# Kernel tuning notes

Hardware: AMD Instinct MI355X
Metric: run time of the kernel (lower is better)

The kernel has to match this reference:

```python
import jax, jax.numpy as jnp
import numpy as np

N_NODES = 40000
N_EDGES = 640000
FEAT_IN = 128
EDGE_FEAT_IN = 16
HID = 128
N_LAYERS = 4
NUM_GRAPHS = 256


def _linear_params(key, fan_in, fan_out):
    k1, k2 = jax.random.split(key)
    s = 1.0 / np.sqrt(fan_in)
    W = jax.random.uniform(k1, (fan_in, fan_out), jnp.float32, -s, s)
    b = jax.random.uniform(k2, (fan_out,), jnp.float32, -s, s)
    return W, b


def setup_inputs() -> dict:
    key = jax.random.key(0)
    ks = jax.random.split(key, 8)
    h = jax.random.normal(ks[0], (N_NODES, FEAT_IN), jnp.float32)
    e = jax.random.normal(ks[1], (N_EDGES, EDGE_FEAT_IN), jnp.float32)
    edge_index = jax.random.randint(ks[2], (2, N_EDGES), 0, N_NODES, jnp.int32)
    batch = jnp.sort(jax.random.randint(ks[3], (N_NODES,), 0, NUM_GRAPHS, jnp.int32))

    W_embed, b_embed = _linear_params(ks[4], FEAT_IN, HID)
    W_eembed, b_eembed = _linear_params(ks[5], EDGE_FEAT_IN, HID)

    layer_keys = jax.random.split(ks[6], N_LAYERS * 3)
    Wm_l, bm_l, Wh_l, bh_l, We_l, be_l = [], [], [], [], [], []
    for i in range(N_LAYERS):
        Wm, bm = _linear_params(layer_keys[3 * i + 0], 3 * HID, HID)
        Wh, bh = _linear_params(layer_keys[3 * i + 1], 2 * HID, HID)
        We, be = _linear_params(layer_keys[3 * i + 2], 3 * HID, HID)
        Wm_l.append(Wm); bm_l.append(bm)
        Wh_l.append(Wh); bh_l.append(bh)
        We_l.append(We); be_l.append(be)

    return {
        "h": h, "e": e, "edge_index": edge_index, "batch": batch,
        "W_embed": W_embed, "b_embed": b_embed,
        "W_eembed": W_eembed, "b_eembed": b_eembed,
        "Wm": jnp.stack(Wm_l), "bm": jnp.stack(bm_l),
        "Wh": jnp.stack(Wh_l), "bh": jnp.stack(bh_l),
        "We": jnp.stack(We_l), "be": jnp.stack(be_l),
    }


def reference(h, e, W_embed, b_embed, W_eembed, b_eembed,
              Wm, bm, Wh, bh, We, be, edge_index, batch):
    send, rec = edge_index[0], edge_index[1]
    h = h @ W_embed + b_embed          # [N, H]
    e = e @ W_eembed + b_eembed        # [E, H]

    def layer(carry, params):
        h, e = carry
        Wm_i, bm_i, Wh_i, bh_i, We_i, be_i = params
        h_send = h[send]               # [E, H] gather
        h_rec = h[rec]                 # [E, H] gather
        cat3 = jnp.concatenate([h_send, h_rec, e], axis=1)  # [E, 3H]
        messages = cat3 @ Wm_i + bm_i                        # [E, H]
        agg = jax.ops.segment_sum(messages, rec, num_segments=N_NODES)  # scatter_add
        h_new = jnp.concatenate([h, agg], axis=1) @ Wh_i + bh_i
        # NOTE: e_update uses h_send/h_rec from the OLD h, as in the source.
        e_new = cat3 @ We_i + be_i
        return (h_new, e_new), None

    (h, e), _ = jax.lax.scan(layer, (h, e), (Wm, bm, Wh, bh, We, be))
    return jax.ops.segment_sum(h, batch, num_segments=NUM_GRAPHS)  # global_add_pool
```

## Files before the change

### kernel.cpp

```cpp
#include <hip/hip_runtime.h>
#include <hip/hip_bf16.h>

#define NN 40000
#define NE 640000
#define NG 256
#define EW 48

typedef __attribute__((ext_vector_type(8))) short bf16x8;
typedef __attribute__((ext_vector_type(4))) float f32x4;

__device__ __forceinline__ unsigned f2b_u(float f){
  unsigned u = __builtin_bit_cast(unsigned, f);
  u += 0x7fffu + ((u >> 16) & 1u);
  return u >> 16;
}
__device__ __forceinline__ float b2f(unsigned short h){
  unsigned u = ((unsigned)h) << 16;
  return __builtin_bit_cast(float, u);
}
__device__ __forceinline__ unsigned scale_pk(unsigned u, float dg){
  float lo = __builtin_bit_cast(float, u << 16);
  float hi = __builtin_bit_cast(float, u & 0xffff0000u);
  return f2b_u(lo * dg) | (f2b_u(hi * dg) << 16);
}

#define LSTRIDE 147456

__global__ __launch_bounds__(256) void pack2_k(
    const float* __restrict__ Wembed, const float* __restrict__ Wh,
    const float* __restrict__ We, unsigned short* __restrict__ wt,
    unsigned short* __restrict__ wp)
{
  __shared__ float T[64][65];
  const int bx = blockIdx.x;
  const int tx = threadIdx.x & 63, ty = threadIdx.x >> 6;
  const float* src; unsigned short* dst; int rowbase, stride, koff, jt, kt;
  if (bx < 4){
    src = Wembed; dst = wt; rowbase = 0; stride = 128; koff = 0;
    kt = bx & 1; jt = bx >> 1;
  } else {
    const int q = bx - 4, l = q / 24, w = q % 24;
    unsigned short* base = wt + 16384 + (size_t)l * LSTRIDE;
    const float* wh = Wh + (size_t)l * 256 * 128;
    const float* we = We + (size_t)l * 384 * 128;
    if (w < 4){       src = wh; rowbase = 0;   dst = base;          stride = 640; koff = 0;   kt = w & 1;        jt = w >> 1; }
    else if (w < 12){ const int u = w - 4;  src = we; rowbase = 128; dst = base + 81920;  stride = 256; koff = 0;   kt = u & 3; jt = u >> 2; }
    else if (w < 16){ const int u = w - 12; src = we; rowbase = 0;   dst = base + 114688; stride = 256; koff = 0;   kt = u & 1; jt = u >> 1; }
    else if (w < 20){ const int u = w - 16; src = we; rowbase = 256; dst = base + 114688; stride = 256; koff = 128; kt = u & 1; jt = u >> 1; }
    else {            const int u = w - 20; src = wh; rowbase = 128; dst = wp + l * 16384; stride = 128; koff = 0; kt = u & 1; jt = u >> 1; }
  }
  const int k0 = kt * 64, j0 = jt * 64;
  #pragma unroll
  for (int rr = 0; rr < 16; ++rr){
    const int r = ty + rr * 4;
    T[r][tx] = src[(size_t)(rowbase + k0 + r) * 128 + j0 + tx];
  }
  __syncthreads();
  #pragma unroll
  for (int rr = 0; rr < 16; ++rr){
    const int j = ty + rr * 4;
    dst[(size_t)(j0 + j) * stride + koff + k0 + tx] = (unsigned short)f2b_u(T[tx][j]);
  }
}

__global__ __launch_bounds__(256, 2) void prodg_k(
    const float* __restrict__ Wm, const unsigned short* __restrict__ wp,
    unsigned short* __restrict__ wt)
{
  __shared__ unsigned short As[128 * 128];
  __shared__ unsigned short Bs[128 * 128];
  const int l = blockIdx.x / 3, pi = blockIdx.x % 3;
  const int rowoff = (pi == 0) ? 128 : (pi == 1) ? 0 : 256;
  const int poff   = (pi == 0) ? 128 : (pi == 1) ? 256 : 384;
  const float* Am = Wm + (size_t)l * 384 * 128 + (size_t)rowoff * 128;
  const unsigned short* Bt = wp + l * 16384;
  unsigned short* base = wt + 16384 + (size_t)l * LSTRIDE;

  const int tid = threadIdx.x;
  const int lane = tid & 63, wave = tid >> 6;
  const int qm = (wave & 1) << 6, qn = (wave >> 1) << 6;
  const int lr = lane & 15, lkc = lane >> 4;
  const int chunk = tid & 15, r0 = tid >> 4;
  f32x4 acc[4][4] = {};

  #pragma unroll
  for (int rr = 0; rr < 8; ++rr){
    const int r = r0 + rr * 16;
    const float* Af = Am + ((size_t)r << 7) + chunk * 8;
    const float4 f0 = *(const float4*)Af;
    const float4 f1 = *(const float4*)(Af + 4);
    uint4 va;
    va.x = f2b_u(f0.x) | (f2b_u(f0.y) << 16);
    va.y = f2b_u(f0.z) | (f2b_u(f0.w) << 16);
    va.z = f2b_u(f1.x) | (f2b_u(f1.y) << 16);
    va.w = f2b_u(f1.z) | (f2b_u(f1.w) << 16);
    *(uint4*)&As[r * 128 + ((chunk ^ (r & 7)) << 3)] = va;
    *(uint4*)&Bs[r * 128 + ((chunk ^ (r & 7)) << 3)] =
        *(const uint4*)(Bt + (size_t)r * 128 + chunk * 8);
  }
  __syncthreads();
  #pragma unroll
  for (int kk = 0; kk < 4; ++kk){
    const int kc = kk * 4 + lkc;
    bf16x8 af[4], bfr[4];
    #pragma unroll
    for (int mi = 0; mi < 4; ++mi){
      const int r = qm + mi * 16 + lr;
      af[mi] = *(const bf16x8*)&As[r * 128 + ((kc ^ (r & 7)) << 3)];
    }
    #pragma unroll
    for (int ni = 0; ni < 4; ++ni){
      const int r = qn + ni * 16 + lr;
      bfr[ni] = *(const bf16x8*)&Bs[r * 128 + ((kc ^ (r & 7)) << 3)];
    }
    #pragma unroll
    for (int mi = 0; mi < 4; ++mi)
      #pragma unroll
      for (int ni = 0; ni < 4; ++ni)
        acc[mi][ni] = __builtin_amdgcn_mfma_f32_16x16x32_bf16(af[mi], bfr[ni], acc[mi][ni], 0, 0, 0);
  }

  const int rbase = (lane >> 4) << 2;
  #pragma unroll
  for (int mi = 0; mi < 4; ++mi){
    #pragma unroll
    for (int r = 0; r < 4; ++r){
      const int gr = qm + mi * 16 + rbase + r;
      #pragma unroll
      for (int ni = 0; ni < 4; ++ni){
        const int col = qn + ni * 16 + lr;
        const unsigned short b = (unsigned short)f2b_u(acc[mi][ni][r]);
        base[(size_t)col * 640 + poff + gr] = b;
        if (pi == 2) base[(size_t)col * 640 + 512 + gr] = b;
      }
    }
  }
}

__global__ __launch_bounds__(1024, 1) void vec2b_k(
    const float* __restrict__ bm, const float* __restrict__ be,
    const unsigned short* __restrict__ wt, const unsigned short* __restrict__ wp,
    float* __restrict__ rw)
{
  __shared__ unsigned short s_wp[16384];
  __shared__ unsigned short s_m3[16384];
  __shared__ unsigned short s_w3[16384];
  __shared__ float c[128], cb[128];
  __shared__ float part_rw[128][8], part_cn[128][8];
  const int t = threadIdx.x;
  const int j = t >> 3, p = t & 7;
  if (t < 128) c[t] = 0.f;

  for (int l = 0; l < 4; ++l){
    const unsigned short* base = wt + 16384 + (size_t)l * LSTRIDE;
    ((uint4*)s_wp)[t]        = ((const uint4*)(wp + l * 16384))[t];
    ((uint4*)s_wp)[t + 1024] = ((const uint4*)(wp + l * 16384))[t + 1024];
    {
      const uint4* srcm = (const uint4*)(base + (size_t)j * 640 + 384);
      ((uint4*)(s_m3 + j * 128))[p * 2]     = srcm[p * 2];
      ((uint4*)(s_m3 + j * 128))[p * 2 + 1] = srcm[p * 2 + 1];
      const uint4* srcw = (const uint4*)(base + 114688 + (size_t)j * 256 + 128);
      ((uint4*)(s_w3 + j * 128))[p * 2]     = srcw[p * 2];
      ((uint4*)(s_w3 + j * 128))[p * 2 + 1] = srcw[p * 2 + 1];
    }
    if (t < 128) cb[t] = bm[l * 128 + t];
    __syncthreads();
    float prw = 0.f, pcn = 0.f;
    #pragma unroll
    for (int q = 0; q < 16; ++q){
      const int kk = p * 16 + q;
      prw += cb[kk] * b2f(s_wp[j * 128 + kk]) + c[kk] * b2f(s_m3[j * 128 + kk]);
      pcn += c[kk] * b2f(s_w3[j * 128 + kk]);
    }
    part_rw[j][p] = prw; part_cn[j][p] = pcn;
    __syncthreads();
    if (t < 128){
      float rwj = 0.f, cnj = be[l * 128 + t];
      #pragma unroll
      for (int i = 0; i < 8; ++i){ rwj += part_rw[t][i]; cnj += part_cn[t][i]; }
      rw[l * 128 + t] = rwj;
      __syncthreads();
      c[t] = cnj;
    } else {
      __syncthreads();
    }
    __syncthreads();
  }
}

struct YCfg {
  const void* A[5];
  const unsigned short* Bt;
  unsigned short* out0;
  const float* bias;
  const float* rv;
  int np;
  int bstride;
  int scale_mask;
};
struct GArgs { YCfg y[3]; };

template<int AT0>
__global__ __launch_bounds__(256, 2) void gemm_multi(
    GArgs ga, int M, const float* __restrict__ degf)
{
  __shared__ unsigned short As[128 * 128];
  __shared__ unsigned short Bs[128 * 128];
  const YCfg c = ga.y[blockIdx.y];
  const int tid = threadIdx.x;
  const int m0 = blockIdx.x * 128;
  const int lane = tid & 63, wave = tid >> 6;
  const int qm = (wave & 1) << 6, qn = (wave >> 1) << 6;
  const int lr = lane & 15, lkc = lane >> 4;
  const int chunk = tid & 15, r0 = tid >> 4;
  f32x4 acc[4][4] = {};

  for (int p = 0; p < c.np; ++p){
    if (p) __syncthreads();
    const unsigned short* Ab = (const unsigned short*)c.A[p];
    const bool scl = (c.scale_mask >> p) & 1;
    #pragma unroll
    for (int rr = 0; rr < 8; ++rr){
      const int r = r0 + rr * 16;
      const int gr = m0 + r;
      uint4 va = make_uint4(0u, 0u, 0u, 0u);
      if (gr < M){
        if (AT0 && p == 0){
          const float* Af = (const float*)c.A[0] + ((size_t)gr << 7) + chunk * 8;
          const float4 f0 = *(const float4*)Af;
          const float4 f1 = *(const float4*)(Af + 4);
          va.x = f2b_u(f0.x) | (f2b_u(f0.y) << 16);
          va.y = f2b_u(f0.z) | (f2b_u(f0.w) << 16);
          va.z = f2b_u(f1.x) | (f2b_u(f1.y) << 16);
          va.w = f2b_u(f1.z) | (f2b_u(f1.w) << 16);
        } else {
          va = *(const uint4*)(Ab + ((size_t)gr << 7) + chunk * 8);
          if (scl){
            const float dg = degf[gr];
            va.x = scale_pk(va.x, dg); va.y = scale_pk(va.y, dg);
            va.z = scale_pk(va.z, dg); va.w = scale_pk(va.w, dg);
          }
        }
      }
      *(uint4*)&As[r * 128 + ((chunk ^ (r & 7)) << 3)] = va;
      *(uint4*)&Bs[r * 128 + ((chunk ^ (r & 7)) << 3)] =
          *(const uint4*)(c.Bt + (size_t)r * c.bstride + p * 128 + chunk * 8);
    }
    __syncthreads();
    #pragma unroll
    for (int kk = 0; kk < 4; ++kk){
      const int kc = kk * 4 + lkc;
      bf16x8 af[4], bfr[4];
      #pragma unroll
      for (int mi = 0; mi < 4; ++mi){
        const int r = qm + mi * 16 + lr;
        af[mi] = *(const bf16x8*)&As[r * 128 + ((kc ^ (r & 7)) << 3)];
      }
      #pragma unroll
      for (int ni = 0; ni < 4; ++ni){
        const int r = qn + ni * 16 + lr;
        bfr[ni] = *(const bf16x8*)&Bs[r * 128 + ((kc ^ (r & 7)) << 3)];
      }
      #pragma unroll
      for (int mi = 0; mi < 4; ++mi)
        #pragma unroll
        for (int ni = 0; ni < 4; ++ni)
          acc[mi][ni] = __builtin_amdgcn_mfma_f32_16x16x32_bf16(af[mi], bfr[ni], acc[mi][ni], 0, 0, 0);
    }
  }

  const int rbase = (lane >> 4) << 2;
  #pragma unroll
  for (int mi = 0; mi < 4; ++mi){
    #pragma unroll
    for (int r = 0; r < 4; ++r){
      const int gr = m0 + qm + mi * 16 + rbase + r;
      if (gr >= M) continue;
      const size_t ro = (size_t)gr << 7;
      float dg = 0.f;
      if (c.rv) dg = degf[gr];
      #pragma unroll
      for (int ni = 0; ni < 4; ++ni){
        const int col = qn + ni * 16 + lr;
        float v = acc[mi][ni][r];
        if (c.bias) v += c.bias[col];
        if (c.rv)   v += dg * c.rv[col];
        c.out0[ro + col] = (unsigned short)f2b_u(v);
      }
    }
  }
}

__global__ void fill_ell_k(const int* __restrict__ rec, const int* __restrict__ send,
                           int* __restrict__ cnt, int2* __restrict__ ell){
  const int i = blockIdx.x * 256 + threadIdx.x;
  if (i < NE){
    const int r = rec[i];
    const int k = atomicAdd(&cnt[r], 1);
    if (k < EW) ell[r * EW + k] = make_int2(send[i], i);
  }
}

__global__ void aux_k(const int* __restrict__ cnt, float* __restrict__ degf,
                      const int* __restrict__ batch, int* __restrict__ gptr){
  const int b = blockIdx.x, t = threadIdx.x;
  if (b < 157){
    const int i = b * 256 + t;
    if (i < NN) degf[i] = (float)cnt[i];
  } else {
    if (t < NG){
      int lo = 0, hi = NN;
      while (lo < hi){
        const int mid = (lo + hi) >> 1;
        if (batch[mid] < t) lo = mid + 1; else hi = mid;
      }
      gptr[t] = lo;
      if (t == 0) gptr[NG] = NN;
    }
  }
}

__global__ __launch_bounds__(256) void sraw_s0_k(
    const int* __restrict__ cnt, const int2* __restrict__ ell,
    const float* __restrict__ e_in, const float* __restrict__ W,
    const float* __restrict__ bias, unsigned short* __restrict__ TPS)
{
  __shared__ float sums[16][16];
  __shared__ float dgs[16];
  __shared__ float Ws[2048];
  __shared__ float bs[128];
  const int t = threadIdx.x;
  const int n0 = blockIdx.x * 16;
  for (int i = t; i < 2048; i += 256) Ws[i] = W[i];
  if (t < 128) bs[t] = bias[t];
  {
    const int a = t >> 4, c16 = t & 15;
    const int n = n0 + a;
    const int m0 = cnt[n];
    const int m = (m0 < EW) ? m0 : EW;
    const int2* row = ell + n * EW;
    float acc = 0.f;
    int j = 0;
    for (; j + 2 <= m; j += 2){
      const int e0 = row[j].y, e1 = row[j + 1].y;
      acc += e_in[(size_t)e0 * 16 + c16] + e_in[(size_t)e1 * 16 + c16];
    }
    if (j < m) acc += e_in[(size_t)row[j].y * 16 + c16];
    sums[a][c16] = acc;
    if (c16 == 0) dgs[a] = (float)m0;
  }
  __syncthreads();
  #pragma unroll
  for (int i = 0; i < 8; ++i){
    const int o = t + 256 * i;
    const int node = o >> 7, col = o & 127;
    float acc = dgs[node] * bs[col];
    #pragma unroll
    for (int k = 0; k < 16; ++k) acc += sums[node][k] * Ws[k * 128 + col];
    TPS[((size_t)(n0 + node) << 7) + col] = (unsigned short)f2b_u(acc);
  }
}

__global__ __launch_bounds__(256) void gather_q_k(
    const int* __restrict__ cnt, const int2* __restrict__ ell,
    const unsigned short* __restrict__ hb, unsigned short* __restrict__ tb)
{
  const int pass = blockIdx.y;
  const int n = blockIdx.x * 4 + (threadIdx.x >> 6);
  const int lane = threadIdx.x & 63;
  const int grp = lane >> 4, l16 = lane & 15;
  const int mc = cnt[n];
  const int m = (mc < EW) ? mc : EW;
  const int idx = (lane < m) ? ell[n * EW + lane].x : 0;
  const unsigned short* cp = hb + pass * 32 + (l16 << 1);
  float a0 = 0.f, a1 = 0.f;
  for (int k = 0; k < m; k += 8){
    const int kk0 = k + grp, kk1 = k + 4 + grp;
    const int s0 = __shfl(idx, kk0 < m ? kk0 : 0);
    const int s1 = __shfl(idx, kk1 < m ? kk1 : 0);
    unsigned v0 = 0u, v1 = 0u;
    if (kk0 < m) v0 = *(const unsigned*)(cp + ((size_t)s0 << 7));
    if (kk1 < m) v1 = *(const unsigned*)(cp + ((size_t)s1 << 7));
    a0 += b2f((unsigned short)(v0 & 0xffffu)) + b2f((unsigned short)(v1 & 0xffffu));
    a1 += b2f((unsigned short)(v0 >> 16)) + b2f((unsigned short)(v1 >> 16));
  }
  a0 += __shfl_xor(a0, 16); a0 += __shfl_xor(a0, 32);
  a1 += __shfl_xor(a1, 16); a1 += __shfl_xor(a1, 32);
  if (grp == 0)
    *(unsigned*)(tb + ((size_t)n << 7) + pass * 32 + (l16 << 1)) =
        f2b_u(a0) | (f2b_u(a1) << 16);
}

__global__ void pool_k(const int* __restrict__ gptr, const unsigned short* __restrict__ hb,
                       float* __restrict__ out)
{
  const int g = blockIdx.x * 4 + (threadIdx.x >> 6);
  const int lane = threadIdx.x & 63;
  float a0 = 0.f, a1 = 0.f;
  for (int n = gptr[g]; n < gptr[g + 1]; ++n){
    const unsigned v = *(const unsigned*)(hb + ((size_t)n << 7) + 2 * lane);
    a0 += b2f((unsigned short)(v & 0xffffu));
    a1 += b2f((unsigned short)(v >> 16));
  }
  float2 r; r.x = a0; r.y = a1;
  *(float2*)(out + (size_t)g * 128 + 2 * lane) = r;
}

extern "C" void kernel_launch(void* const* d_in, const int* in_sizes, int n_in,
                              void* d_out, int out_size, void* d_ws, size_t ws_size,
                              hipStream_t stream)
{
  const float* h_in     = (const float*)d_in[0];
  const float* e_in     = (const float*)d_in[1];
  const int*   eidx     = (const int*)d_in[2];
  const int*   batch    = (const int*)d_in[3];
  const float* W_embed  = (const float*)d_in[4];
  const float* b_embed  = (const float*)d_in[5];
  const float* W_eembed = (const float*)d_in[6];
  const float* b_eembed = (const float*)d_in[7];
  const float* Wm       = (const float*)d_in[8];
  const float* bm       = (const float*)d_in[9];
  const float* Wh       = (const float*)d_in[10];
  const float* bh       = (const float*)d_in[11];
  const float* We       = (const float*)d_in[12];
  const float* be       = (const float*)d_in[13];
  const int* send = eidx;
  const int* rec  = eidx + NE;

  char* ws = (char*)d_ws;
  size_t off = 0;
  auto alloc = [&](size_t bytes) -> char* {
    char* p = ws + off;
    off = (off + bytes + 255) & ~(size_t)255;
    return p;
  };
  unsigned short* wt  = (unsigned short*)alloc((size_t)(16384 + 4 * LSTRIDE) * 2);
  unsigned short* wp  = (unsigned short*)alloc((size_t)4 * 16384 * 2);
  unsigned short* hA  = (unsigned short*)alloc((size_t)NN * 128 * 2);
  unsigned short* hB  = (unsigned short*)alloc((size_t)NN * 128 * 2);
  unsigned short* Q0  = (unsigned short*)alloc((size_t)NN * 128 * 2);
  unsigned short* Q1  = (unsigned short*)alloc((size_t)NN * 128 * 2);
  unsigned short* T0  = (unsigned short*)alloc((size_t)NN * 128 * 2);
  unsigned short* T1  = (unsigned short*)alloc((size_t)NN * 128 * 2);
  unsigned short* tb  = (unsigned short*)alloc((size_t)NN * 128 * 2);
  float* rw   = (float*)alloc((size_t)512 * 4);
  int* cnt    = (int*)alloc((size_t)NN * 4);
  float* degf = (float*)alloc((size_t)NN * 4);
  int* gptr   = (int*)alloc((size_t)(NG + 1) * 4);
  int2* ell   = (int2*)alloc((size_t)NN * EW * 8);

  if (off > ws_size) return;

  const dim3 B256(256);

  pack2_k<<<dim3(100), B256, 0, stream>>>(W_embed, Wh, We, wt, wp);
  prodg_k<<<dim3(12), B256, 0, stream>>>(Wm, wp, wt);
  vec2b_k<<<dim3(1), dim3(1024), 0, stream>>>(bm, be, wt, wp, rw);

  hipMemsetAsync(cnt, 0, (size_t)NN * 4, stream);
  fill_ell_k<<<dim3(2500), B256, 0, stream>>>(rec, send, cnt, ell);
  aux_k<<<dim3(158), B256, 0, stream>>>(cnt, degf, batch, gptr);
  sraw_s0_k<<<dim3(NN / 16), B256, 0, stream>>>(cnt, ell, e_in, W_eembed, b_eembed, T0);

  {
    GArgs ga = {};
    ga.y[0].A[0] = h_in; ga.y[0].Bt = wt; ga.y[0].out0 = hA;
    ga.y[0].bias = b_embed; ga.y[0].np = 1; ga.y[0].bstride = 128;
    ga.y[0].scale_mask = 0;
    gemm_multi<1><<<dim3(313, 1), B256, 0, stream>>>(ga, NN, degf);
  }

  unsigned short* hc = hA;  unsigned short* hn = hB;
  unsigned short* Qc = Q0;  unsigned short* Qn = Q1;
  unsigned short* Tc = T0;  unsigned short* Tn = T1;
  for (int l = 0; l < 4; ++l){
    const unsigned short* LB = wt + 16384 + (size_t)l * LSTRIDE;

    gather_q_k<<<dim3(NN / 4, 4), B256, 0, stream>>>(cnt, ell, hc, tb);

    GArgs ga = {};
    YCfg& y0 = ga.y[0];
    y0.A[0] = hc; y0.A[1] = hc; y0.A[2] = tb; y0.A[3] = Tc; y0.A[4] = Qc;
    y0.Bt = LB; y0.out0 = hn; y0.bias = bh + l * 128; y0.rv = rw + l * 128;
    y0.np = (l == 0) ? 4 : 5;
    y0.bstride = 640; y0.scale_mask = (1 << 1) | (1 << 4);
    int ny = 1;
    if (l < 3){
      YCfg& y1 = ga.y[1];
      y1.A[0] = hc; y1.A[1] = Qc; y1.Bt = LB + 81920;
      y1.out0 = Qn; y1.np = (l == 0) ? 1 : 2; y1.bstride = 256; y1.scale_mask = 0;
      YCfg& y2 = ga.y[2];
      y2.A[0] = tb; y2.A[1] = Tc; y2.Bt = LB + 114688;
      y2.out0 = Tn; y2.np = 2; y2.bstride = 256; y2.scale_mask = 0;
      ny = 3;
    }
    gemm_multi<0><<<dim3(313, ny), B256, 0, stream>>>(ga, NN, degf);

    unsigned short* t2;
    t2 = hc; hc = hn; hn = t2;
    t2 = Qc; Qc = Qn; Qn = t2;
    t2 = Tc; Tc = Tn; Tn = t2;
  }

  pool_k<<<dim3(NG / 4), B256, 0, stream>>>(gptr, hc, (float*)d_out);
}
```

Baseline: 697.2 us.

## Prearrange weights into MFMA fragment layout and drop shared-memory B staging

Adds a one-off kernel that copies weight panels into a fragment-ordered layout, so the GEMM reads B operands directly from global memory (L1/L2-resident) instead of staging them in LDS. Degree scaling of A tiles is replaced by a second accumulator for the same A tile, applied as dg*(acc2+rv) in the epilogue. This removes half the LDS footprint and the per-stage scale conversions, and cuts the number of A tile loads (hc loaded once for two weight blocks). In exchange, each wave issues global loads for B inside the MFMA loop, and a second accumulator array doubles accumulator register use, which can hurt occupancy.

Result: slower. 738.5 us (+5.9%).

```diff
diff --git a/kernel.cpp b/kernel.cpp
--- a/kernel.cpp
+++ b/kernel.cpp
@@ -17,11 +17,6 @@
 __device__ __forceinline__ float b2f(unsigned short h){
   unsigned u = ((unsigned)h) << 16;
   return __builtin_bit_cast(float, u);
-}
-__device__ __forceinline__ unsigned scale_pk(unsigned u, float dg){
-  float lo = __builtin_bit_cast(float, u << 16);
-  float hi = __builtin_bit_cast(float, u & 0xffff0000u);
-  return f2b_u(lo * dg) | (f2b_u(hi * dg) << 16);
 }
 
 #define LSTRIDE 147456
@@ -137,6 +132,26 @@
   }
 }
 
+__global__ void frag_k(const unsigned short* __restrict__ wt,
+                       unsigned short* __restrict__ wf)
+{
+  const int gp = blockIdx.y;
+  const int g = blockIdx.x * 256 + threadIdx.x;
+  const int kc = g >> 7, r = g & 127;
+  const unsigned short* src; unsigned short* dst; int bstride, p;
+  if (gp == 0){ src = wt; dst = wf; bstride = 128; p = 0; }
+  else {
+    const int q = gp - 1, l = q / 9, w = q % 9;
+    const unsigned short* sb = wt + 16384 + (size_t)l * LSTRIDE;
+    dst = wf + 16384 + (size_t)l * LSTRIDE + w * 16384;
+    if (w < 5){      src = sb;           bstride = 640; p = w; }
+    else if (w < 7){ src = sb + 81920;   bstride = 256; p = w - 5; }
+    else {           src = sb + 114688;  bstride = 256; p = w - 7; }
+  }
+  *(uint4*)(dst + (size_t)g * 8) =
+      *(const uint4*)(src + (size_t)r * bstride + p * 128 + kc * 8);
+}
+
 __global__ __launch_bounds__(1024, 1) void vec2b_k(
     const float* __restrict__ bm, const float* __restrict__ be,
     const unsigned short* __restrict__ wt, const unsigned short* __restrict__ wp,
@@ -188,24 +203,16 @@
   }
 }
 
-struct YCfg {
-  const void* A[5];
-  const unsigned short* Bt;
-  unsigned short* out0;
-  const float* bias;
-  const float* rv;
-  int np;
-  int bstride;
-  int scale_mask;
-};
+struct Stg { const void* A; int nb; int bo[2]; int bt[2]; };
+struct YCfg { Stg s[4]; int ns; unsigned short* out0; const float* bias; const float* rv; };
 struct GArgs { YCfg y[3]; };
 
 template<int AT0>
 __global__ __launch_bounds__(256, 2) void gemm_multi(
-    GArgs ga, int M, const float* __restrict__ degf)
+    GArgs ga, int M, const float* __restrict__ degf,
+    const unsigned short* __restrict__ wf)
 {
   __shared__ unsigned short As[128 * 128];
-  __shared__ unsigned short Bs[128 * 128];
   const YCfg c = ga.y[blockIdx.y];
   const int tid = threadIdx.x;
   const int m0 = blockIdx.x * 128;
@@ -213,20 +220,20 @@
   const int qm = (wave & 1) << 6, qn = (wave >> 1) << 6;
   const int lr = lane & 15, lkc = lane >> 4;
   const int chunk = tid & 15, r0 = tid >> 4;
-  f32x4 acc[4][4] = {};
-
-  for (int p = 0; p < c.np; ++p){
-    if (p) __syncthreads();
-    const unsigned short* Ab = (const unsigned short*)c.A[p];
-    const bool scl = (c.scale_mask >> p) & 1;
+  f32x4 ac1[4][4] = {};
+  f32x4 ac2[4][4] = {};
+
+  for (int s = 0; s < c.ns; ++s){
+    if (s) __syncthreads();
+    const Stg st = c.s[s];
     #pragma unroll
     for (int rr = 0; rr < 8; ++rr){
       const int r = r0 + rr * 16;
       const int gr = m0 + r;
       uint4 va = make_uint4(0u, 0u, 0u, 0u);
       if (gr < M){
-        if (AT0 && p == 0){
-          const float* Af = (const float*)c.A[0] + ((size_t)gr << 7) + chunk * 8;
+        if (AT0 && s == 0){
+          const float* Af = (const float*)st.A + ((size_t)gr << 7) + chunk * 8;
           const float4 f0 = *(const float4*)Af;
           const float4 f1 = *(const float4*)(Af + 4);
           va.x = f2b_u(f0.x) | (f2b_u(f0.y) << 16);
@@ -234,38 +241,40 @@
           va.z = f2b_u(f1.x) | (f2b_u(f1.y) << 16);
           va.w = f2b_u(f1.z) | (f2b_u(f1.w) << 16);
         } else {
-          va = *(const uint4*)(Ab + ((size_t)gr << 7) + chunk * 8);
-          if (scl){
-            const float dg = degf[gr];
-            va.x = scale_pk(va.x, dg); va.y = scale_pk(va.y, dg);
-            va.z = scale_pk(va.z, dg); va.w = scale_pk(va.w, dg);
-          }
+          va = *(const uint4*)((const unsigned short*)st.A + ((size_t)gr << 7) + chunk * 8);
         }
       }
       *(uint4*)&As[r * 128 + ((chunk ^ (r & 7)) << 3)] = va;
-      *(uint4*)&Bs[r * 128 + ((chunk ^ (r & 7)) << 3)] =
-          *(const uint4*)(c.Bt + (size_t)r * c.bstride + p * 128 + chunk * 8);
     }
     __syncthreads();
     #pragma unroll
     for (int kk = 0; kk < 4; ++kk){
       const int kc = kk * 4 + lkc;
-      bf16x8 af[4], bfr[4];
+      bf16x8 af[4];
       #pragma unroll
       for (int mi = 0; mi < 4; ++mi){
         const int r = qm + mi * 16 + lr;
         af[mi] = *(const bf16x8*)&As[r * 128 + ((kc ^ (r & 7)) << 3)];
       }
-      #pragma unroll
-      for (int ni = 0; ni < 4; ++ni){
-        const int r = qn + ni * 16 + lr;
-        bfr[ni] = *(const bf16x8*)&Bs[r * 128 + ((kc ^ (r & 7)) << 3)];
+      for (int b = 0; b < st.nb; ++b){
+        const bf16x8* bp = (const bf16x8*)(wf + st.bo[b]) + kc * 128 + qn + lr;
+        bf16x8 bfr[4];
+        #pragma unroll
+        for (int ni = 0; ni < 4; ++ni) bfr[ni] = bp[ni * 16];
+        if (st.bt[b] == 0){
+          #pragma unroll
+          for (int mi = 0; mi < 4; ++mi)
+            #pragma unroll
+            for (int ni = 0; ni < 4; ++ni)
+              ac1[mi][ni] = __builtin_amdgcn_mfma_f32_16x16x32_bf16(af[mi], bfr[ni], ac1[mi][ni], 0, 0, 0);
+        } else {
+          #pragma unroll
+          for (int mi = 0; mi < 4; ++mi)
+            #pragma unroll
+            for (int ni = 0; ni < 4; ++ni)
+              ac2[mi][ni] = __builtin_amdgcn_mfma_f32_16x16x32_bf16(af[mi], bfr[ni], ac2[mi][ni], 0, 0, 0);
+        }
       }
-      #pragma unroll
-      for (int mi = 0; mi < 4; ++mi)
-        #pragma unroll
-        for (int ni = 0; ni < 4; ++ni)
-          acc[mi][ni] = __builtin_amdgcn_mfma_f32_16x16x32_bf16(af[mi], bfr[ni], acc[mi][ni], 0, 0, 0);
     }
   }
 
@@ -282,9 +291,9 @@
       #pragma unroll
       for (int ni = 0; ni < 4; ++ni){
         const int col = qn + ni * 16 + lr;
-        float v = acc[mi][ni][r];
+        float v = ac1[mi][ni][r];
         if (c.bias) v += c.bias[col];
-        if (c.rv)   v += dg * c.rv[col];
+        if (c.rv)   v += dg * (ac2[mi][ni][r] + c.rv[col]);
         c.out0[ro + col] = (unsigned short)f2b_u(v);
       }
     }
@@ -435,6 +444,7 @@
     return p;
   };
   unsigned short* wt  = (unsigned short*)alloc((size_t)(16384 + 4 * LSTRIDE) * 2);
+  unsigned short* wf  = (unsigned short*)alloc((size_t)(16384 + 4 * LSTRIDE) * 2);
   unsigned short* wp  = (unsigned short*)alloc((size_t)4 * 16384 * 2);
   unsigned short* hA  = (unsigned short*)alloc((size_t)NN * 128 * 2);
   unsigned short* hB  = (unsigned short*)alloc((size_t)NN * 128 * 2);
@@ -455,6 +465,7 @@
 
   pack2_k<<<dim3(100), B256, 0, stream>>>(W_embed, Wh, We, wt, wp);
   prodg_k<<<dim3(12), B256, 0, stream>>>(Wm, wp, wt);
+  frag_k<<<dim3(8, 37), B256, 0, stream>>>(wt, wf);
   vec2b_k<<<dim3(1), dim3(1024), 0, stream>>>(bm, be, wt, wp, rw);
 
   hipMemsetAsync(cnt, 0, (size_t)NN * 4, stream);
@@ -464,37 +475,48 @@
 
   {
     GArgs ga = {};
-    ga.y[0].A[0] = h_in; ga.y[0].Bt = wt; ga.y[0].out0 = hA;
-    ga.y[0].bias = b_embed; ga.y[0].np = 1; ga.y[0].bstride = 128;
-    ga.y[0].scale_mask = 0;
-    gemm_multi<1><<<dim3(313, 1), B256, 0, stream>>>(ga, NN, degf);
+    YCfg& y = ga.y[0];
+    y.s[0].A = h_in; y.s[0].nb = 1; y.s[0].bo[0] = 0; y.s[0].bt[0] = 0;
+    y.ns = 1; y.out0 = hA; y.bias = b_embed; y.rv = nullptr;
+    gemm_multi<1><<<dim3(313, 1), B256, 0, stream>>>(ga, NN, degf, wf);
   }
 
   unsigned short* hc = hA;  unsigned short* hn = hB;
   unsigned short* Qc = Q0;  unsigned short* Qn = Q1;
   unsigned short* Tc = T0;  unsigned short* Tn = T1;
   for (int l = 0; l < 4; ++l){
-    const unsigned short* LB = wt + 16384 + (size_t)l * LSTRIDE;
+    const int LB = 16384 + l * LSTRIDE;
 
     gather_q_k<<<dim3(NN / 4, 4), B256, 0, stream>>>(cnt, ell, hc, tb);
 
     GArgs ga = {};
     YCfg& y0 = ga.y[0];
-    y0.A[0] = hc; y0.A[1] = hc; y0.A[2] = tb; y0.A[3] = Tc; y0.A[4] = Qc;
-    y0.Bt = LB; y0.out0 = hn; y0.bias = bh + l * 128; y0.rv = rw + l * 128;
-    y0.np = (l == 0) ? 4 : 5;
-    y0.bstride = 640; y0.scale_mask = (1 << 1) | (1 << 4);
+    y0.s[0].A = hc; y0.s[0].nb = 2;
+    y0.s[0].bo[0] = LB;          y0.s[0].bt[0] = 0;
+    y0.s[0].bo[1] = LB + 16384;  y0.s[0].bt[1] = 1;
+    y0.s[1].A = tb; y0.s[1].nb = 1;
+    y0.s[1].bo[0] = LB + 32768;  y0.s[1].bt[0] = 0;
+    y0.s[2].A = Tc; y0.s[2].nb = 1;
+    y0.s[2].bo[0] = LB + 49152;  y0.s[2].bt[0] = 0;
+    y0.s[3].A = Qc; y0.s[3].nb = 1;
+    y0.s[3].bo[0] = LB + 65536;  y0.s[3].bt[0] = 1;
+    y0.ns = (l == 0) ? 3 : 4;
+    y0.out0 = hn; y0.bias = bh + l * 128; y0.rv = rw + l * 128;
     int ny = 1;
     if (l < 3){
       YCfg& y1 = ga.y[1];
-      y1.A[0] = hc; y1.A[1] = Qc; y1.Bt = LB + 81920;
-      y1.out0 = Qn; y1.np = (l == 0) ? 1 : 2; y1.bstride = 256; y1.scale_mask = 0;
+      y1.s[0].A = hc; y1.s[0].nb = 1; y1.s[0].bo[0] = LB + 81920; y1.s[0].bt[0] = 0;
+      y1.s[1].A = Qc; y1.s[1].nb = 1; y1.s[1].bo[0] = LB + 98304; y1.s[1].bt[0] = 0;
+      y1.ns = (l == 0) ? 1 : 2;
+      y1.out0 = Qn; y1.bias = nullptr; y1.rv = nullptr;
       YCfg& y2 = ga.y[2];
-      y2.A[0] = tb; y2.A[1] = Tc; y2.Bt = LB + 114688;
-      y2.out0 = Tn; y2.np = 2; y2.bstride = 256; y2.scale_mask = 0;
+      y2.s[0].A = tb; y2.s[0].nb = 1; y2.s[0].bo[0] = LB + 114688; y2.s[0].bt[0] = 0;
+      y2.s[1].A = Tc; y2.s[1].nb = 1; y2.s[1].bo[0] = LB + 131072; y2.s[1].bt[0] = 0;
+      y2.ns = 2;
+      y2.out0 = Tn; y2.bias = nullptr; y2.rv = nullptr;
       ny = 3;
     }
-    gemm_multi<0><<<dim3(313, ny), B256, 0, stream>>>(ga, NN, degf);
+    gemm_multi<0><<<dim3(313, ny), B256, 0, stream>>>(ga, NN, degf, wf);
 
     unsigned short* t2;
     t2 = hc; hc = hn; hn = t2;
```

## Split ELL into separate sender/edge arrays and gather full rows per wave

Applied to the files above, without the earlier changes.

The interleaved int2 ELL table becomes two int arrays, sender indices and edge ids, with the edge-id array aliased onto the tb buffer that is only needed later. The gather kernel drops its 4-pass blockIdx.y split. Each wavefront now reads a whole 256-byte node row using 8-byte loads per lane, two neighbours per wave step, unrolled 16 neighbours deep. This reads the index list once instead of four times, issues wider loads and exposes more memory-level parallelism, at the cost of more registers and the reliance on tb being overwritten only after sraw_s0_k consumes ell_e.

Result: faster. 599.4 us (-14.0%).

```diff
diff --git a/kernel.cpp b/kernel.cpp
--- a/kernel.cpp
+++ b/kernel.cpp
@@ -292,12 +292,16 @@
 }
 
 __global__ void fill_ell_k(const int* __restrict__ rec, const int* __restrict__ send,
-                           int* __restrict__ cnt, int2* __restrict__ ell){
+                           int* __restrict__ cnt, int* __restrict__ ell_s,
+                           int* __restrict__ ell_e){
   const int i = blockIdx.x * 256 + threadIdx.x;
   if (i < NE){
     const int r = rec[i];
     const int k = atomicAdd(&cnt[r], 1);
-    if (k < EW) ell[r * EW + k] = make_int2(send[i], i);
+    if (k < EW){
+      ell_s[r * EW + k] = send[i];
+      ell_e[r * EW + k] = i;
+    }
   }
 }
 
@@ -321,7 +325,7 @@
 }
 
 __global__ __launch_bounds__(256) void sraw_s0_k(
-    const int* __restrict__ cnt, const int2* __restrict__ ell,
+    const int* __restrict__ cnt, const int* __restrict__ ell_e,
     const float* __restrict__ e_in, const float* __restrict__ W,
     const float* __restrict__ bias, unsigned short* __restrict__ TPS)
 {
@@ -338,14 +342,14 @@
     const int n = n0 + a;
     const int m0 = cnt[n];
     const int m = (m0 < EW) ? m0 : EW;
-    const int2* row = ell + n * EW;
+    const int* row = ell_e + n * EW;
     float acc = 0.f;
     int j = 0;
     for (; j + 2 <= m; j += 2){
-      const int e0 = row[j].y, e1 = row[j + 1].y;
+      const int e0 = row[j], e1 = row[j + 1];
       acc += e_in[(size_t)e0 * 16 + c16] + e_in[(size_t)e1 * 16 + c16];
     }
-    if (j < m) acc += e_in[(size_t)row[j].y * 16 + c16];
+    if (j < m) acc += e_in[(size_t)row[j] * 16 + c16];
     sums[a][c16] = acc;
     if (c16 == 0) dgs[a] = (float)m0;
   }
@@ -361,34 +365,62 @@
   }
 }
 
-__global__ __launch_bounds__(256) void gather_q_k(
-    const int* __restrict__ cnt, const int2* __restrict__ ell,
+__global__ __launch_bounds__(256) void gather_k(
+    const int* __restrict__ cnt, const int* __restrict__ ell_s,
     const unsigned short* __restrict__ hb, unsigned short* __restrict__ tb)
 {
-  const int pass = blockIdx.y;
   const int n = blockIdx.x * 4 + (threadIdx.x >> 6);
   const int lane = threadIdx.x & 63;
-  const int grp = lane >> 4, l16 = lane & 15;
+  const int half = lane >> 5, l32 = lane & 31;
   const int mc = cnt[n];
   const int m = (mc < EW) ? mc : EW;
-  const int idx = (lane < m) ? ell[n * EW + lane].x : 0;
-  const unsigned short* cp = hb + pass * 32 + (l16 << 1);
-  float a0 = 0.f, a1 = 0.f;
-  for (int k = 0; k < m; k += 8){
-    const int kk0 = k + grp, kk1 = k + 4 + grp;
-    const int s0 = __shfl(idx, kk0 < m ? kk0 : 0);
-    const int s1 = __shfl(idx, kk1 < m ? kk1 : 0);
-    unsigned v0 = 0u, v1 = 0u;
-    if (kk0 < m) v0 = *(const unsigned*)(cp + ((size_t)s0 << 7));
-    if (kk1 < m) v1 = *(const unsigned*)(cp + ((size_t)s1 << 7));
-    a0 += b2f((unsigned short)(v0 & 0xffffu)) + b2f((unsigned short)(v1 & 0xffffu));
-    a1 += b2f((unsigned short)(v0 >> 16)) + b2f((unsigned short)(v1 >> 16));
-  }
-  a0 += __shfl_xor(a0, 16); a0 += __shfl_xor(a0, 32);
-  a1 += __shfl_xor(a1, 16); a1 += __shfl_xor(a1, 32);
-  if (grp == 0)
-    *(unsigned*)(tb + ((size_t)n << 7) + pass * 32 + (l16 << 1)) =
-        f2b_u(a0) | (f2b_u(a1) << 16);
+  const unsigned short* colp = hb + 4 * l32;
+  const int myidx = (lane < m) ? ell_s[n * EW + lane] : 0;
+  float a0 = 0.f, a1 = 0.f, a2 = 0.f, a3 = 0.f;
+  int k = 0;
+  for (; k + 16 <= m; k += 16){
+    int s[8];
+    #pragma unroll
+    for (int u = 0; u < 8; ++u) s[u] = __shfl(myidx, k + 2 * u + half);
+    uint2 v[8];
+    #pragma unroll
+    for (int u = 0; u < 8; ++u) v[u] = *(const uint2*)(colp + ((size_t)s[u] << 7));
+    #pragma unroll
+    for (int u = 0; u < 8; ++u){
+      a0 += b2f((unsigned short)(v[u].x & 0xffffu));
+      a1 += b2f((unsigned short)(v[u].x >> 16));
+      a2 += b2f((unsigned short)(v[u].y & 0xffffu));
+      a3 += b2f((unsigned short)(v[u].y >> 16));
+    }
+  }
+  for (; k + 4 <= m; k += 4){
+    const int s0 = __shfl(myidx, k + half);
+    const int s1 = __shfl(myidx, k + 2 + half);
+    const uint2 v0 = *(const uint2*)(colp + ((size_t)s0 << 7));
+    const uint2 v1 = *(const uint2*)(colp + ((size_t)s1 << 7));
+    a0 += b2f((unsigned short)(v0.x & 0xffffu)) + b2f((unsigned short)(v1.x & 0xffffu));
+    a1 += b2f((unsigned short)(v0.x >> 16)) + b2f((unsigned short)(v1.x >> 16));
+    a2 += b2f((unsigned short)(v0.y & 0xffffu)) + b2f((unsigned short)(v1.y & 0xffffu));
+    a3 += b2f((unsigned short)(v0.y >> 16)) + b2f((unsigned short)(v1.y >> 16));
+  }
+  for (; k < m; k += 2){
+    if (k + half < m){
+      const int s = __shfl(myidx, k + half);
+      const uint2 v = *(const uint2*)(colp + ((size_t)s << 7));
+      a0 += b2f((unsigned short)(v.x & 0xffffu));
+      a1 += b2f((unsigned short)(v.x >> 16));
+      a2 += b2f((unsigned short)(v.y & 0xffffu));
+      a3 += b2f((unsigned short)(v.y >> 16));
+    }
+  }
+  a0 += __shfl_xor(a0, 32); a1 += __shfl_xor(a1, 32);
+  a2 += __shfl_xor(a2, 32); a3 += __shfl_xor(a3, 32);
+  if (half == 0){
+    uint2 o;
+    o.x = f2b_u(a0) | (f2b_u(a1) << 16);
+    o.y = f2b_u(a2) | (f2b_u(a3) << 16);
+    *(uint2*)(tb + ((size_t)n << 7) + 4 * l32) = o;
+  }
 }
 
 __global__ void pool_k(const int* __restrict__ gptr, const unsigned short* __restrict__ hb,
@@ -447,7 +479,8 @@
   int* cnt    = (int*)alloc((size_t)NN * 4);
   float* degf = (float*)alloc((size_t)NN * 4);
   int* gptr   = (int*)alloc((size_t)(NG + 1) * 4);
-  int2* ell   = (int2*)alloc((size_t)NN * EW * 8);
+  int* ell_s  = (int*)alloc((size_t)NN * EW * 4);
+  int* ell_e  = (int*)tb;
 
   if (off > ws_size) return;
 
@@ -458,9 +491,9 @@
   vec2b_k<<<dim3(1), dim3(1024), 0, stream>>>(bm, be, wt, wp, rw);
 
   hipMemsetAsync(cnt, 0, (size_t)NN * 4, stream);
-  fill_ell_k<<<dim3(2500), B256, 0, stream>>>(rec, send, cnt, ell);
+  fill_ell_k<<<dim3(2500), B256, 0, stream>>>(rec, send, cnt, ell_s, ell_e);
   aux_k<<<dim3(158), B256, 0, stream>>>(cnt, degf, batch, gptr);
-  sraw_s0_k<<<dim3(NN / 16), B256, 0, stream>>>(cnt, ell, e_in, W_eembed, b_eembed, T0);
+  sraw_s0_k<<<dim3(NN / 16), B256, 0, stream>>>(cnt, ell_e, e_in, W_eembed, b_eembed, T0);
 
   {
     GArgs ga = {};
@@ -476,7 +509,7 @@
   for (int l = 0; l < 4; ++l){
     const unsigned short* LB = wt + 16384 + (size_t)l * LSTRIDE;
 
-    gather_q_k<<<dim3(NN / 4, 4), B256, 0, stream>>>(cnt, ell, hc, tb);
+    gather_k<<<dim3(NN / 4), B256, 0, stream>>>(cnt, ell_s, hc, tb);
 
     GArgs ga = {};
     YCfg& y0 = ga.y[0];
```
